# Kernel tuning notes

Hardware: AMD Instinct MI355X
Metric: run time of the kernel (lower is better)

Reference implementation:

```python
import jax, jax.numpy as jnp
import numpy as np

N = 100000      # nodes
E = 800000      # directed edges
D_IN = 128      # input features (n_inputs)
HIDDEN = 128    # conf['model']['hidden_size']
D_OUT = 2       # conv2 output classes


def setup_inputs() -> dict:
    key = jax.random.key(0)
    k0, k1, k2, k3 = jax.random.split(key, 4)
    x = jax.random.normal(k0, (N, D_IN), dtype=jnp.float32)
    edge_index = jax.random.randint(k1, (2, E), 0, N, dtype=jnp.int32)
    # Glorot-style init for GCNConv weights, zero bias (PyG defaults)
    s1 = float(np.sqrt(6.0 / (D_IN + HIDDEN)))
    s2 = float(np.sqrt(6.0 / (HIDDEN + D_OUT)))
    W1 = jax.random.uniform(k2, (D_IN, HIDDEN), jnp.float32, -s1, s1)
    b1 = jnp.zeros((HIDDEN,), jnp.float32)
    W2 = jax.random.uniform(k3, (HIDDEN, D_OUT), jnp.float32, -s2, s2)
    b2 = jnp.zeros((D_OUT,), jnp.float32)
    return {"x": x, "edge_index": edge_index, "W1": W1, "b1": b1, "W2": W2, "b2": b2}


def gcn_conv(x, src, dst, W, b):
    """PyG GCNConv: add self-loops, symmetric deg^-1/2 A deg^-1/2 normalization."""
    n = x.shape[0]
    h = x @ W                                                   # [N, F_out]
    ones_e = jnp.ones((src.shape[0],), h.dtype)
    # degree with self-loops (init to 1)
    deg = jnp.ones((n,), h.dtype).at[dst].add(ones_e)           # [N]
    dinv = 1.0 / jnp.sqrt(deg)
    norm = (dinv[src] * dinv[dst])[:, None]                     # [E, 1]
    # self-loop contribution: norm_ii = dinv_i^2; then scatter edge messages
    out = (h * (dinv * dinv)[:, None]).at[dst].add(h[src] * norm)
    return out + b


def reference(x, edge_index, W1, b1, W2, b2):
    src, dst = edge_index[0], edge_index[1]
    h = jax.nn.relu(gcn_conv(x, src, dst, W1, b1))
    return gcn_conv(h, src, dst, W2, b2)                        # [N, 2]
```

## Files before the change

kernel.cpp:

```cpp
#include <hip/hip_runtime.h>
#include <hip/hip_bf16.h>


#define D1 128
#define BSH 9
#define BSZ (1 << BSH)
#define CHA 4096

typedef __attribute__((ext_vector_type(8))) short short8;
typedef __attribute__((ext_vector_type(4))) float floatx4;

__device__ __forceinline__ unsigned short f2bf(float f) {
    unsigned u = __float_as_uint(f);
    u += 0x7fff + ((u >> 16) & 1);
    return (unsigned short)(u >> 16);
}
__device__ __forceinline__ float bflo(unsigned u) { return __uint_as_float(u << 16); }
__device__ __forceinline__ float bfhi(unsigned u) { return __uint_as_float(u & 0xffff0000u); }

__global__ void k_init(const float* __restrict__ W1, unsigned short* __restrict__ W1t,
                       int* __restrict__ bcount) {
    int i = blockIdx.x * 256 + threadIdx.x;
    if (i < 256) bcount[i] = 0;
    if (i < D1 * D1) {
        int c = i >> 7, k = i & 127;
        W1t[c * D1 + k] = f2bf(W1[k * D1 + c]);
    }
}

__global__ __launch_bounds__(256) void k_bcount(const int* __restrict__ dst,
                                                int* __restrict__ bcount,
                                                int E, int nbuck) {
    __shared__ int h[256];
    int t = threadIdx.x;
    h[t] = 0;
    __syncthreads();
    for (int i = blockIdx.x * 256 + t; i < E; i += gridDim.x * 256)
        atomicAdd(&h[dst[i] >> BSH], 1);
    __syncthreads();
    if (t < nbuck && h[t]) atomicAdd(&bcount[t], h[t]);
}

__global__ __launch_bounds__(256) void k_bscan(const int* __restrict__ bcount,
                                               int* __restrict__ bbase,
                                               int* __restrict__ bcur,
                                               int* __restrict__ rowptr,
                                               int nbuck, int N, int E) {
    __shared__ int sd[256];
    int t = threadIdx.x;
    int v = (t < nbuck) ? bcount[t] : 0;
    sd[t] = v;
    __syncthreads();
    for (int off = 1; off < 256; off <<= 1) {
        int x = (t >= off) ? sd[t - off] : 0;
        __syncthreads();
        sd[t] += x;
        __syncthreads();
    }
    int excl = sd[t] - v;
    if (t < nbuck) { bbase[t] = excl; bcur[t] = excl; }
    if (t == 0) {
        bbase[nbuck] = E;
        rowptr[N] = E;
    }
}

__global__ __launch_bounds__(256) void k_binA(
    const int* __restrict__ src, const int* __restrict__ dst,
    int* __restrict__ bcur, unsigned* __restrict__ packed, int E, int nbuck)
{
    __shared__ int hist[256];
    __shared__ int cur[256];
    const int t = threadIdx.x;
    const int e0 = blockIdx.x * CHA;
    const int e1 = min(e0 + CHA, E);

    for (int i = t; i < nbuck; i += 256) hist[i] = 0;
    __syncthreads();
    for (int i = e0 + t; i < e1; i += 256)
        atomicAdd(&hist[dst[i] >> BSH], 1);
    __syncthreads();
    for (int i = t; i < nbuck; i += 256)
        cur[i] = (hist[i] > 0) ? atomicAdd(&bcur[i], hist[i]) : 0;
    __syncthreads();
    for (int i = e0 + t; i < e1; i += 256) {
        int d = dst[i];
        int b = d >> BSH;
        int pos = atomicAdd(&cur[b], 1);
        packed[pos] = ((unsigned)src[i] << BSH) | (unsigned)(d & (BSZ - 1));
    }
}

__global__ __launch_bounds__(512) void k_binB(
    const int* __restrict__ bbase, const unsigned* __restrict__ packed,
    int* __restrict__ rowptr, float* __restrict__ dinv,
    int* __restrict__ esrc, int* __restrict__ order, int N)
{
    __shared__ int lh[BSZ];
    __shared__ int sd[BSZ];
    __shared__ int lcur[BSZ];
    __shared__ int dbin[64];
    __shared__ int dcur[64];

    const int t = threadIdx.x;
    const int s = blockIdx.x << BSH;
    const int n = min(BSZ, N - s);
    const int base = bbase[blockIdx.x];
    const int cnt = bbase[blockIdx.x + 1] - base;

    lh[t] = 0;
    if (t < 64) dbin[t] = 0;
    __syncthreads();
    for (int i = t; i < cnt; i += 512)
        atomicAdd(&lh[packed[base + i] & (BSZ - 1)], 1);
    __syncthreads();

    sd[t] = lh[t];
    __syncthreads();
    for (int off = 1; off < BSZ; off <<= 1) {
        int x = (t >= off) ? sd[t - off] : 0;
        __syncthreads();
        sd[t] += x;
        __syncthreads();
    }
    int excl = sd[t] - lh[t];
    if (t < n) {
        rowptr[s + t] = base + excl;
        dinv[s + t] = rsqrtf(1.0f + (float)lh[t]);
        atomicAdd(&dbin[63 - min(lh[t], 63)], 1);
    }
    lcur[t] = excl;
    __syncthreads();

    for (int i = t; i < cnt; i += 512) {
        unsigned p = packed[base + i];
        int ld = (int)(p & (BSZ - 1));
        int pos = atomicAdd(&lcur[ld], 1);
        esrc[base + pos] = (int)(p >> BSH);
    }

    __syncthreads();
    if (t < 64) sd[t] = dbin[t];
    __syncthreads();
    for (int off = 1; off < 64; off <<= 1) {
        int x = (t >= off && t < 64) ? sd[t - off] : 0;
        __syncthreads();
        if (t < 64) sd[t] += x;
        __syncthreads();
    }
    if (t < 64) dcur[t] = sd[t] - dbin[t];
    __syncthreads();
    if (t < n) {
        int b = 63 - min(lh[t], 63);
        int pos = atomicAdd(&dcur[b], 1);
        order[s + pos] = s + t;
    }
}

#define BMM 64
__global__ __launch_bounds__(256) void k_gemm1(
    const float* __restrict__ x, const unsigned short* __restrict__ W1t,
    const float* __restrict__ dinv, unsigned short* __restrict__ h1s, int N)
{
    __shared__ unsigned short Xs[BMM][136];
    __shared__ unsigned short Ws[D1][136];

    const int t = threadIdx.x;
    const int row0 = blockIdx.x * BMM;

#pragma unroll
    for (int i = 0; i < 8; ++i) {
        int idx = t + 256 * i;
        int r = idx >> 4, c8 = idx & 15;
        short8 v = ((const short8*)W1t)[r * 16 + c8];
        *(short8*)&Ws[r][c8 * 8] = v;
    }
#pragma unroll
    for (int i = 0; i < 4; ++i) {
        int idx = t + 256 * i;
        int r = idx >> 4, c8 = idx & 15;
        int row = row0 + r;
        short8 v8 = (short8)0;
        if (row < N) {
            const float* p = x + (size_t)row * D1 + c8 * 8;
            float4 f0 = *(const float4*)p;
            float4 f1 = *(const float4*)(p + 4);
            v8[0] = (short)f2bf(f0.x); v8[1] = (short)f2bf(f0.y);
            v8[2] = (short)f2bf(f0.z); v8[3] = (short)f2bf(f0.w);
            v8[4] = (short)f2bf(f1.x); v8[5] = (short)f2bf(f1.y);
            v8[6] = (short)f2bf(f1.z); v8[7] = (short)f2bf(f1.w);
        }
        *(short8*)&Xs[r][c8 * 8] = v8;
    }
    __syncthreads();

    const int w = t >> 6;
    const int l = t & 63;
    const int m = l & 15;
    const int q = l >> 4;

    floatx4 acc[8];
#pragma unroll
    for (int c = 0; c < 8; ++c) acc[c] = (floatx4)0.0f;

#pragma unroll
    for (int ks = 0; ks < 4; ++ks) {
        short8 a = *(const short8*)&Xs[16 * w + m][ks * 32 + q * 8];
#pragma unroll
        for (int c = 0; c < 8; ++c) {
            short8 b = *(const short8*)&Ws[c * 16 + m][ks * 32 + q * 8];
            acc[c] = __builtin_amdgcn_mfma_f32_16x16x32_bf16(a, b, acc[c], 0, 0, 0);
        }
    }

#pragma unroll
    for (int r = 0; r < 4; ++r) {
        int row = row0 + 16 * w + q * 4 + r;
        if (row >= N) continue;
        float di = dinv[row];
#pragma unroll
        for (int c = 0; c < 8; ++c)
            h1s[(size_t)row * D1 + c * 16 + m] = f2bf(acc[c][r] * di);
    }
}

#define ACC8(A, v) \
    A[0] += bflo(v.x); A[1] += bfhi(v.x); \
    A[2] += bflo(v.y); A[3] += bfhi(v.y); \
    A[4] += bflo(v.z); A[5] += bfhi(v.z); \
    A[6] += bflo(v.w); A[7] += bfhi(v.w);

__global__ __launch_bounds__(256) void k_agg1_gemm2(
    const int* __restrict__ rowptr, const int* __restrict__ esrc,
    const int* __restrict__ order,
    const float* __restrict__ dinv, const unsigned short* __restrict__ h1s,
    const float* __restrict__ b1, const float* __restrict__ W2,
    float* __restrict__ h2s, int N)
{
    int gid = blockIdx.x * 256 + threadIdx.x;
    int grp = gid >> 4;
    if (grp >= N) return;
    int node = order[grp];
    int lane = gid & 15;

    const uint4* h1v = (const uint4*)h1s;

    uint4 u = h1v[(size_t)node * 16 + lane];
    float accA[8], accB[8];
    accA[0] = bflo(u.x); accA[1] = bfhi(u.x);
    accA[2] = bflo(u.y); accA[3] = bfhi(u.y);
    accA[4] = bflo(u.z); accA[5] = bfhi(u.z);
    accA[6] = bflo(u.w); accA[7] = bfhi(u.w);
#pragma unroll
    for (int j = 0; j < 8; ++j) accB[j] = 0.f;

    int beg = rowptr[node], end = rowptr[node + 1];
    int e = beg;
    for (; e + 7 < end; e += 8) {
        int s0 = esrc[e],     s1 = esrc[e + 1], s2 = esrc[e + 2], s3 = esrc[e + 3];
        int s4 = esrc[e + 4], s5 = esrc[e + 5], s6 = esrc[e + 6], s7 = esrc[e + 7];
        uint4 v0 = h1v[(size_t)s0 * 16 + lane];
        uint4 v1 = h1v[(size_t)s1 * 16 + lane];
        uint4 v2 = h1v[(size_t)s2 * 16 + lane];
        uint4 v3 = h1v[(size_t)s3 * 16 + lane];
        uint4 v4 = h1v[(size_t)s4 * 16 + lane];
        uint4 v5 = h1v[(size_t)s5 * 16 + lane];
        uint4 v6 = h1v[(size_t)s6 * 16 + lane];
        uint4 v7 = h1v[(size_t)s7 * 16 + lane];
        ACC8(accA, v0) ACC8(accB, v1) ACC8(accA, v2) ACC8(accB, v3)
        ACC8(accA, v4) ACC8(accB, v5) ACC8(accA, v6) ACC8(accB, v7)
    }
    if (e + 3 < end) {
        int s0 = esrc[e], s1 = esrc[e + 1], s2 = esrc[e + 2], s3 = esrc[e + 3];
        uint4 v0 = h1v[(size_t)s0 * 16 + lane];
        uint4 v1 = h1v[(size_t)s1 * 16 + lane];
        uint4 v2 = h1v[(size_t)s2 * 16 + lane];
        uint4 v3 = h1v[(size_t)s3 * 16 + lane];
        ACC8(accA, v0) ACC8(accB, v1) ACC8(accA, v2) ACC8(accB, v3)
        e += 4;
    }
    for (; e < end; ++e) {
        uint4 v = h1v[(size_t)esrc[e] * 16 + lane];
        ACC8(accB, v)
    }

    float di = dinv[node];
    const float4* b1v = (const float4*)b1;
    float4 bbA = b1v[lane * 2 + 0];
    float4 bbB = b1v[lane * 2 + 1];
    float a[8];
    a[0] = fmaxf((accA[0] + accB[0]) * di + bbA.x, 0.f);
    a[1] = fmaxf((accA[1] + accB[1]) * di + bbA.y, 0.f);
    a[2] = fmaxf((accA[2] + accB[2]) * di + bbA.z, 0.f);
    a[3] = fmaxf((accA[3] + accB[3]) * di + bbA.w, 0.f);
    a[4] = fmaxf((accA[4] + accB[4]) * di + bbB.x, 0.f);
    a[5] = fmaxf((accA[5] + accB[5]) * di + bbB.y, 0.f);
    a[6] = fmaxf((accA[6] + accB[6]) * di + bbB.z, 0.f);
    a[7] = fmaxf((accA[7] + accB[7]) * di + bbB.w, 0.f);

    const float4* W2v = (const float4*)W2;
    float p0 = 0.f, p1 = 0.f;
#pragma unroll
    for (int j2 = 0; j2 < 4; ++j2) {
        float4 wv = W2v[lane * 4 + j2];
        p0 += a[j2 * 2] * wv.x + a[j2 * 2 + 1] * wv.z;
        p1 += a[j2 * 2] * wv.y + a[j2 * 2 + 1] * wv.w;
    }

#pragma unroll
    for (int off = 8; off > 0; off >>= 1) {
        p0 += __shfl_xor(p0, off);
        p1 += __shfl_xor(p1, off);
    }
    if (lane == 0) {
        h2s[(size_t)node * 2 + 0] = p0 * di;
        h2s[(size_t)node * 2 + 1] = p1 * di;
    }
}

__global__ void k_gather2(const int* __restrict__ rowptr, const int* __restrict__ esrc,
                          const float* __restrict__ h2s, const float* __restrict__ dinv,
                          const float* __restrict__ b2, float* __restrict__ out, int N)
{
    int i = blockIdx.x * 256 + threadIdx.x;
    if (i >= N) return;
    const float2* h2v = (const float2*)h2s;
    float2 h = h2v[i];
    float o0a = h.x, o1a = h.y;
    float o0b = 0.f, o1b = 0.f;
    int beg = rowptr[i], end = rowptr[i + 1];
    int e = beg;
    for (; e + 7 < end; e += 8) {
        int s0 = esrc[e],     s1 = esrc[e + 1], s2 = esrc[e + 2], s3 = esrc[e + 3];
        int s4 = esrc[e + 4], s5 = esrc[e + 5], s6 = esrc[e + 6], s7 = esrc[e + 7];
        float2 v0 = h2v[s0], v1 = h2v[s1], v2 = h2v[s2], v3 = h2v[s3];
        float2 v4 = h2v[s4], v5 = h2v[s5], v6 = h2v[s6], v7 = h2v[s7];
        o0a += v0.x + v2.x + v4.x + v6.x; o1a += v0.y + v2.y + v4.y + v6.y;
        o0b += v1.x + v3.x + v5.x + v7.x; o1b += v1.y + v3.y + v5.y + v7.y;
    }
    for (; e < end; ++e) {
        float2 v = h2v[esrc[e]];
        o0b += v.x; o1b += v.y;
    }
    float di = dinv[i];
    ((float2*)out)[i] = make_float2((o0a + o0b) * di + b2[0], (o1a + o1b) * di + b2[1]);
}

extern "C" void kernel_launch(void* const* d_in, const int* in_sizes, int n_in,
                              void* d_out, int out_size, void* d_ws, size_t ws_size,
                              hipStream_t stream)
{
    const float* x  = (const float*)d_in[0];
    const int*   ei = (const int*)d_in[1];
    const float* W1 = (const float*)d_in[2];
    const float* b1 = (const float*)d_in[3];
    const float* W2 = (const float*)d_in[4];
    const float* b2 = (const float*)d_in[5];
    float* out = (float*)d_out;

    const int N = in_sizes[0] / D1;
    const int E = in_sizes[1] / 2;
    const int* src = ei;
    const int* dst = ei + E;

    char* w = (char*)d_ws;
    auto alloc = [&](size_t bytes) -> char* {
        char* r = w;
        w += (bytes + 15) & ~(size_t)15;
        return r;
    };
    unsigned short* h1s = (unsigned short*)alloc((size_t)N * D1 * 2);
    unsigned short* W1t = (unsigned short*)alloc((size_t)D1 * D1 * 2);
    float* h2s    = (float*)alloc((size_t)N * 2 * 4);
    float* dinv   = (float*)alloc((size_t)N * 4);
    int*   rowptr = (int*)alloc((size_t)(N + 4) * 4);
    int*   order  = (int*)alloc((size_t)N * 4);
    int*   bcount = (int*)alloc(256 * 4);
    int*   bbase  = (int*)alloc(260 * 4);
    int*   bcur   = (int*)alloc(256 * 4);
    unsigned* packed = (unsigned*)alloc((size_t)E * 4);
    int*   esrc   = (int*)alloc((size_t)E * 4);

    const int nbuck = (N + BSZ - 1) >> BSH;

    k_init  <<<(D1 * D1 + 255) / 256, 256, 0, stream>>>(W1, W1t, bcount);
    k_bcount<<<256, 256, 0, stream>>>(dst, bcount, E, nbuck);
    k_bscan <<<1, 256, 0, stream>>>(bcount, bbase, bcur, rowptr, nbuck, N, E);
    k_binA  <<<(E + CHA - 1) / CHA, 256, 0, stream>>>(src, dst, bcur, packed, E, nbuck);
    k_binB  <<<nbuck, 512, 0, stream>>>(bbase, packed, rowptr, dinv, esrc, order, N);

    k_gemm1<<<(N + BMM - 1) / BMM, 256, 0, stream>>>(x, W1t, dinv, h1s, N);

    k_agg1_gemm2<<<(N * 16 + 255) / 256, 256, 0, stream>>>(rowptr, esrc, order, dinv, h1s, b1, W2, h2s, N);

    k_gather2<<<(N + 255) / 256, 256, 0, stream>>>(rowptr, esrc, h2s, dinv, b2, out, N);
}
```

Baseline: 199.7 us.

## Split h1 into four feature slices for cache-friendly gather aggregation

The layer-1 GEMM now writes h1 as four 32-feature slices, each stored contiguously across all nodes. The aggregation kernel handles one slice per block with 4 lanes per node, so each gather pass works over a smaller (≈6.4MB) slice that fits better in L2/MALL. Per-slice partial W2 products go to a scratch buffer, and a new reduction kernel sums them and applies dinv. The cost is four passes over the edge index list, one extra kernel launch and extra scratch traffic.

Result: slower. 206.0 us (+3.2%).

```diff
diff --git a/kernel.cpp b/kernel.cpp
--- a/kernel.cpp
+++ b/kernel.cpp
@@ -220,7 +220,7 @@
         float di = dinv[row];
 #pragma unroll
         for (int c = 0; c < 8; ++c)
-            h1s[(size_t)row * D1 + c * 16 + m] = f2bf(acc[c][r] * di);
+            h1s[((size_t)(c >> 1) * N + row) * 32 + (c & 1) * 16 + m] = f2bf(acc[c][r] * di);
     }
 }
 
@@ -230,22 +230,24 @@
     A[4] += bflo(v.z); A[5] += bfhi(v.z); \
     A[6] += bflo(v.w); A[7] += bfhi(v.w);
 
-__global__ __launch_bounds__(256) void k_agg1_gemm2(
+__global__ __launch_bounds__(256) void k_agg1(
     const int* __restrict__ rowptr, const int* __restrict__ esrc,
     const int* __restrict__ order,
     const float* __restrict__ dinv, const unsigned short* __restrict__ h1s,
     const float* __restrict__ b1, const float* __restrict__ W2,
-    float* __restrict__ h2s, int N)
-{
-    int gid = blockIdx.x * 256 + threadIdx.x;
-    int grp = gid >> 4;
+    float2* __restrict__ hp, int N)
+{
+    const int slice = blockIdx.x & 3;
+    const int chunk = blockIdx.x >> 2;
+    const int t = threadIdx.x;
+    const int grp = chunk * 64 + (t >> 2);
     if (grp >= N) return;
-    int node = order[grp];
-    int lane = gid & 15;
-
-    const uint4* h1v = (const uint4*)h1s;
-
-    uint4 u = h1v[(size_t)node * 16 + lane];
+    const int lane = t & 3;
+    const int node = order[grp];
+
+    const uint4* hv = (const uint4*)h1s + (size_t)slice * N * 4;
+
+    uint4 u = hv[(size_t)node * 4 + lane];
     float accA[8], accB[8];
     accA[0] = bflo(u.x); accA[1] = bfhi(u.x);
     accA[2] = bflo(u.y); accA[3] = bfhi(u.y);
@@ -259,35 +261,36 @@
     for (; e + 7 < end; e += 8) {
         int s0 = esrc[e],     s1 = esrc[e + 1], s2 = esrc[e + 2], s3 = esrc[e + 3];
         int s4 = esrc[e + 4], s5 = esrc[e + 5], s6 = esrc[e + 6], s7 = esrc[e + 7];
-        uint4 v0 = h1v[(size_t)s0 * 16 + lane];
-        uint4 v1 = h1v[(size_t)s1 * 16 + lane];
-        uint4 v2 = h1v[(size_t)s2 * 16 + lane];
-        uint4 v3 = h1v[(size_t)s3 * 16 + lane];
-        uint4 v4 = h1v[(size_t)s4 * 16 + lane];
-        uint4 v5 = h1v[(size_t)s5 * 16 + lane];
-        uint4 v6 = h1v[(size_t)s6 * 16 + lane];
-        uint4 v7 = h1v[(size_t)s7 * 16 + lane];
+        uint4 v0 = hv[(size_t)s0 * 4 + lane];
+        uint4 v1 = hv[(size_t)s1 * 4 + lane];
+        uint4 v2 = hv[(size_t)s2 * 4 + lane];
+        uint4 v3 = hv[(size_t)s3 * 4 + lane];
+        uint4 v4 = hv[(size_t)s4 * 4 + lane];
+        uint4 v5 = hv[(size_t)s5 * 4 + lane];
+        uint4 v6 = hv[(size_t)s6 * 4 + lane];
+        uint4 v7 = hv[(size_t)s7 * 4 + lane];
         ACC8(accA, v0) ACC8(accB, v1) ACC8(accA, v2) ACC8(accB, v3)
         ACC8(accA, v4) ACC8(accB, v5) ACC8(accA, v6) ACC8(accB, v7)
     }
     if (e + 3 < end) {
         int s0 = esrc[e], s1 = esrc[e + 1], s2 = esrc[e + 2], s3 = esrc[e + 3];
-        uint4 v0 = h1v[(size_t)s0 * 16 + lane];
-        uint4 v1 = h1v[(size_t)s1 * 16 + lane];
-        uint4 v2 = h1v[(size_t)s2 * 16 + lane];
-        uint4 v3 = h1v[(size_t)s3 * 16 + lane];
+        uint4 v0 = hv[(size_t)s0 * 4 + lane];
+        uint4 v1 = hv[(size_t)s1 * 4 + lane];
+        uint4 v2 = hv[(size_t)s2 * 4 + lane];
+        uint4 v3 = hv[(size_t)s3 * 4 + lane];
         ACC8(accA, v0) ACC8(accB, v1) ACC8(accA, v2) ACC8(accB, v3)
         e += 4;
     }
     for (; e < end; ++e) {
-        uint4 v = h1v[(size_t)esrc[e] * 16 + lane];
+        uint4 v = hv[(size_t)esrc[e] * 4 + lane];
         ACC8(accB, v)
     }
 
     float di = dinv[node];
+    const int f0 = slice * 32 + lane * 8;
     const float4* b1v = (const float4*)b1;
-    float4 bbA = b1v[lane * 2 + 0];
-    float4 bbB = b1v[lane * 2 + 1];
+    float4 bbA = b1v[f0 >> 2];
+    float4 bbB = b1v[(f0 >> 2) + 1];
     float a[8];
     a[0] = fmaxf((accA[0] + accB[0]) * di + bbA.x, 0.f);
     a[1] = fmaxf((accA[1] + accB[1]) * di + bbA.y, 0.f);
@@ -302,20 +305,29 @@
     float p0 = 0.f, p1 = 0.f;
 #pragma unroll
     for (int j2 = 0; j2 < 4; ++j2) {
-        float4 wv = W2v[lane * 4 + j2];
+        float4 wv = W2v[(f0 >> 1) + j2];
         p0 += a[j2 * 2] * wv.x + a[j2 * 2 + 1] * wv.z;
         p1 += a[j2 * 2] * wv.y + a[j2 * 2 + 1] * wv.w;
     }
-
-#pragma unroll
-    for (int off = 8; off > 0; off >>= 1) {
-        p0 += __shfl_xor(p0, off);
-        p1 += __shfl_xor(p1, off);
-    }
-    if (lane == 0) {
-        h2s[(size_t)node * 2 + 0] = p0 * di;
-        h2s[(size_t)node * 2 + 1] = p1 * di;
-    }
+    p0 += __shfl_xor(p0, 1); p1 += __shfl_xor(p1, 1);
+    p0 += __shfl_xor(p0, 2); p1 += __shfl_xor(p1, 2);
+    if (lane == 0) hp[(size_t)slice * N + grp] = make_float2(p0, p1);
+}
+
+__global__ void k_h2red(const float2* __restrict__ hp, const int* __restrict__ order,
+                        const float* __restrict__ dinv, float* __restrict__ h2s, int N)
+{
+    int g = blockIdx.x * 256 + threadIdx.x;
+    if (g >= N) return;
+    float p0 = 0.f, p1 = 0.f;
+#pragma unroll
+    for (int s = 0; s < 4; ++s) {
+        float2 v = hp[(size_t)s * N + g];
+        p0 += v.x; p1 += v.y;
+    }
+    int node = order[g];
+    float di = dinv[node];
+    ((float2*)h2s)[node] = make_float2(p0 * di, p1 * di);
 }
 
 __global__ void k_gather2(const int* __restrict__ rowptr, const int* __restrict__ esrc,
@@ -366,12 +378,13 @@
     char* w = (char*)d_ws;
     auto alloc = [&](size_t bytes) -> char* {
         char* r = w;
-        w += (bytes + 15) & ~(size_t)15;
+        w += (bytes + 63) & ~(size_t)63;
         return r;
     };
     unsigned short* h1s = (unsigned short*)alloc((size_t)N * D1 * 2);
     unsigned short* W1t = (unsigned short*)alloc((size_t)D1 * D1 * 2);
     float* h2s    = (float*)alloc((size_t)N * 2 * 4);
+    float2* hp    = (float2*)alloc((size_t)N * 4 * 8);
     float* dinv   = (float*)alloc((size_t)N * 4);
     int*   rowptr = (int*)alloc((size_t)(N + 4) * 4);
     int*   order  = (int*)alloc((size_t)N * 4);
@@ -391,7 +404,9 @@
 
     k_gemm1<<<(N + BMM - 1) / BMM, 256, 0, stream>>>(x, W1t, dinv, h1s, N);
 
-    k_agg1_gemm2<<<(N * 16 + 255) / 256, 256, 0, stream>>>(rowptr, esrc, order, dinv, h1s, b1, W2, h2s, N);
+    const int nchunk = (N + 63) / 64;
+    k_agg1 <<<nchunk * 4, 256, 0, stream>>>(rowptr, esrc, order, dinv, h1s, b1, W2, hp, N);
+    k_h2red<<<(N + 255) / 256, 256, 0, stream>>>(hp, order, dinv, h2s, N);
 
     k_gather2<<<(N + 255) / 256, 256, 0, stream>>>(rowptr, esrc, h2s, dinv, b2, out, N);
 }
```
